# Kernel optimization log

Hardware: AMD Instinct MI355X
Metric: run time of the kernel (lower is better)

## Reference

```python
import jax, jax.numpy as jnp
import numpy as np

C = 512          # in_channels
N1 = 8192        # level-1 nodes
N2 = 131072      # level-2 nodes
N = 1 + N1 + N2  # total nodes (node 0 = root)
E = 1_000_000    # edges
STEP = 10        # ceil(1/ratio), ratio=0.1
K1 = (N1 + STEP - 1) // STEP   # 820 level-1 clusters
K2 = 4 * K1                    # max level-2 clusters (4 centers per parent)
M = 1 + K1 + K2                # coarse node count


def setup_inputs() -> dict:
    key = jax.random.key(0)
    ks = jax.random.split(key, 6)
    x = jax.random.normal(ks[0], (N, C), dtype=jnp.float32)
    edge_index = jax.random.randint(ks[1], (2, E), 0, N, dtype=jnp.int32)
    # fixed hierarchy layout: node 0 root, nodes 1..N1 level-1, rest level-2
    node_type = jnp.concatenate([jnp.zeros(1, jnp.int32),
                                 jnp.ones(N1, jnp.int32),
                                 jnp.full((N2,), 2, jnp.int32)])
    # tree: level-2 nodes point to a level-1 parent (global idx in [1, N1])
    tree = jax.random.randint(ks[2], (N,), 1, N1 + 1, dtype=jnp.int32)
    x_y_index = jax.random.uniform(ks[3], (N, 2), dtype=jnp.float32) * 100.0
    weight_1 = jax.random.normal(ks[4], (1, C), dtype=jnp.float32) * 0.04
    weight_2 = jax.random.normal(ks[5], (1, C), dtype=jnp.float32) * 0.04
    return {"x": x, "edge_index": edge_index, "node_type": node_type,
            "tree": tree, "x_y_index": x_y_index,
            "weight_1": weight_1, "weight_2": weight_2}


def _pair_dist(a, b):
    # a:[m,3], b:[n,3]; xy euclidean distance + |fitness diff| (euclidean_dist)
    dxy = jnp.sqrt(jnp.sum((a[:, None, :2] - b[None, :, :2]) ** 2, axis=-1))
    df = jnp.abs(a[:, None, 2] - b[None, :, 2])
    return dxy + df


def reference(x, edge_index, node_type, tree, x_y_index, weight_1, weight_2):
    x1, x2 = x[1:1 + N1], x[1 + N1:]
    xy1, xy2 = x_y_index[1:1 + N1], x_y_index[1 + N1:]

    # ---- level-1: fitness, threshold selection, cluster by nearest center ----
    f1 = jnp.tanh(jnp.sum(x1 * weight_1, axis=-1) / jnp.linalg.norm(weight_1))
    xyf1 = jnp.concatenate([xy1, f1[:, None]], axis=-1)          # [N1,3]
    order1 = jnp.argsort(f1)
    thr1 = order1[::STEP]                                        # [K1]
    d1 = _pair_dist(xyf1[thr1], xyf1)                            # [K1,N1]
    cluster_1 = jnp.argmin(d1, axis=0).astype(jnp.int32)         # [N1]

    # ---- level-2: fitness, 4 centers per parent cluster, nearest-center ----
    f2 = jnp.tanh(jnp.sum(x2 * weight_2, axis=-1) / jnp.linalg.norm(weight_2))
    xyf2 = jnp.concatenate([xy2, f2[:, None]], axis=-1)          # [N2,3]
    tree2 = tree[1 + N1:]
    parents = cluster_1[tree2 - jnp.min(tree2)]                  # [N2] in [0,K1)
    # pick 4 lowest-fitness members of each parent cluster as centers
    # (static-shape deterministic variant of random.sample over sorted fitness)
    comp_key = parents.astype(jnp.float32) * 4.0 + f2            # fitness in (-1,1)
    order2 = jnp.argsort(comp_key)
    p_sorted = parents[order2]
    counts = jax.ops.segment_sum(jnp.ones((N2,), jnp.int32), parents, K1)
    starts = jnp.concatenate([jnp.zeros(1, jnp.int32), jnp.cumsum(counts)[:-1]])
    rank = jnp.arange(N2, dtype=jnp.int32) - starts[p_sorted]
    row = jnp.where(rank < 4, p_sorted, K1)                      # overflow -> dummy row
    cand = jnp.full((K1 + 1, 4), -1, jnp.int32)
    cand = cand.at[row, jnp.clip(rank, 0, 3)].set(order2.astype(jnp.int32))[:K1]
    valid = cand >= 0                                            # [K1,4]
    cand_xyf = xyf2[jnp.where(valid, cand, 0)]                   # [K1,4,3]
    a = cand_xyf[parents]                                        # [N2,4,3]
    d2 = (jnp.sqrt(jnp.sum((a[..., :2] - xy2[:, None, :]) ** 2, axis=-1))
          + jnp.abs(a[..., 2] - f2[:, None]))
    d2 = jnp.where(valid[parents], d2, jnp.inf)
    local = jnp.argmin(d2, axis=1).astype(jnp.int32)             # [N2] in [0,4)
    cluster_2 = parents * 4 + local                              # [N2]

    # ---- merge cluster ids: [root | level-1 clusters | level-2 clusters] ----
    cluster = jnp.concatenate([jnp.zeros(1, jnp.int32),
                               cluster_1 + 1,
                               cluster_2 + 1 + K1])              # [N] in [0,M)

    # ---- scatter-mean pooling of features and coordinates ----
    cnt = jnp.maximum(jax.ops.segment_sum(jnp.ones((N, 1), x.dtype), cluster, M), 1.0)
    x_pool = jax.ops.segment_sum(x, cluster, M) / cnt            # [M,C]
    new_xy = jax.ops.segment_sum(x_y_index, cluster, M) / cnt    # [M,2]

    # ---- coarsen adjacency (self loops added on fine graph first) ----
    rows = jnp.concatenate([edge_index[0], jnp.arange(N, dtype=jnp.int32)])
    cols = jnp.concatenate([edge_index[1], jnp.arange(N, dtype=jnp.int32)])
    A = jnp.zeros((M, M), x.dtype).at[cluster[rows], cluster[cols]].add(1.0)

    new_node_type = jnp.concatenate([jnp.zeros(1, jnp.int32),
                                     jnp.ones(K1, jnp.int32),
                                     jnp.full((K2,), 2, jnp.int32)])
    new_tree = jnp.concatenate([jnp.full((1,), -1, jnp.int32),
                                jnp.zeros(K1, jnp.int32),
                                jnp.repeat(jnp.arange(1, K1 + 1, dtype=jnp.int32), 4)])
    fitness = jnp.concatenate([jnp.zeros(1, x.dtype), f1, f2])
    batch = jnp.zeros((M,), jnp.int32)
    return x_pool, A, batch, cluster, new_node_type, new_tree, fitness, new_xy
```

## Files before the change

kernel.cpp:

```cpp
#include <hip/hip_runtime.h>
#include <cstdint>
#include <cstddef>
#include <math.h>

#define C_     512
#define N1_    8192
#define N2_    131072
#define NTOT   139265
#define E_     1000000
#define K1_    820
#define K2_    3280
#define M_     4101
#define NB2    256
#define NBM    273

#define OFF_XPOOL   0ull
#define OFF_A       2099712ull
#define OFF_BATCH   18917913ull
#define OFF_CLUSTER 18922014ull
#define OFF_NNT     19061279ull
#define OFF_NTREE   19065380ull
#define OFF_FIT     19069481ull
#define OFF_NXY     19208746ull
#define OUT_TOTAL   19216948ull


__global__ void k_zero4(float4* __restrict__ p, long n4, float* __restrict__ tail, int ntail) {
    long i = (long)blockIdx.x * blockDim.x + threadIdx.x;
    long stride = (long)gridDim.x * blockDim.x;
    float4 z = make_float4(0.f, 0.f, 0.f, 0.f);
    for (; i < n4; i += stride) p[i] = z;
    if (blockIdx.x == 0 && threadIdx.x < ntail) tail[threadIdx.x] = 0.f;
}

__device__ __forceinline__ float pairwise_combine(float r) {
    float o;
    o = __shfl_xor(r, 1, 64);  r = __fadd_rn(r, o);
    o = __shfl_xor(r, 2, 64);  r = __fadd_rn(r, o);
    o = __shfl_xor(r, 4, 64);  r = __fadd_rn(r, o);
    o = __shfl_xor(r, 8, 64);  r = __fadd_rn(r, o);
    o = __shfl_xor(r, 16, 64); r = __fadd_rn(r, o);
    return r;
}

__global__ void k_norms(const float* __restrict__ w1, const float* __restrict__ w2,
                        float* __restrict__ norms) {
    __shared__ float buf[2][C_];
    int wv = threadIdx.x >> 6, lane = threadIdx.x & 63;
    const float* w = (wv == 0) ? w1 : w2;
    float4* b4 = (float4*)buf[wv];
    const float4* w4 = (const float4*)w;
    b4[lane] = w4[lane];
    b4[lane + 64] = w4[lane + 64];
    __syncthreads();
    float r = 0.f;
    if (lane < 32) {
        int base = (lane >> 3) * 128 + (lane & 7);
        float v = buf[wv][base];
        r = __fmul_rn(v, v);
        for (int i = 1; i < 16; ++i) {
            float u = buf[wv][base + 8 * i];
            r = __fadd_rn(r, __fmul_rn(u, u));
        }
    }
    r = pairwise_combine(r);
    if (lane == 0) norms[wv] = __fsqrt_rn(r);
}

__global__ void k_fit(const float* __restrict__ x, const float* __restrict__ w,
                      const float* __restrict__ norms, int normIdx,
                      int rowOff, int nRows, float* __restrict__ fs,
                      float* __restrict__ fitOut) {
    __shared__ float wbuf[C_];
    __shared__ float xbuf[4][C_];
    for (int j = threadIdx.x; j < C_; j += 256) wbuf[j] = w[j];
    int wv = threadIdx.x >> 6, lane = threadIdx.x & 63;
    int gw = blockIdx.x * 4 + wv;
    const float4* row = (const float4*)(x + (size_t)(rowOff + gw) * C_);
    float4* xb4 = (float4*)xbuf[wv];
    xb4[lane] = row[lane];
    xb4[lane + 64] = row[lane + 64];
    __syncthreads();
    float r = 0.f;
    if (lane < 32) {
        int base = (lane >> 3) * 128 + (lane & 7);
        r = __fmul_rn(xbuf[wv][base], wbuf[base]);
        for (int i = 1; i < 16; ++i) {
            int c = base + 8 * i;
            r = __fadd_rn(r, __fmul_rn(xbuf[wv][c], wbuf[c]));
        }
    }
    r = pairwise_combine(r);
    if (lane == 0) {
        float q = __fdiv_rn(r, norms[normIdx]);
        float f = (float)tanh((double)q);
        fs[gw] = f;
        fitOut[gw] = f;
    }
    (void)nRows;
}

#define RJ 512
__global__ void k_rank_partial(const float* __restrict__ f1s, int* __restrict__ rank) {
    __shared__ float buf[RJ];
    int i = blockIdx.x * 256 + threadIdx.x;
    int jbase = blockIdx.y * RJ;
    for (int j = threadIdx.x; j < RJ; j += 256) buf[j] = f1s[jbase + j];
    float fi = f1s[i];
    __syncthreads();
    int r = 0;
    #pragma unroll 8
    for (int j = 0; j < RJ; ++j) {
        float fj = buf[j];
        int jj = jbase + j;
        r += (int)((fj < fi) || (fj == fi && jj < i));
    }
    atomicAdd(&rank[i], r);
}

__global__ void k_thr_emit(const int* __restrict__ rank, int* __restrict__ thr1) {
    int i = blockIdx.x * blockDim.x + threadIdx.x;
    if (i >= N1_) return;
    int r = rank[i];
    if (r % 10 == 0) thr1[r / 10] = i;
}

__global__ void k_thr_gather(const int* __restrict__ thr1, const float* __restrict__ xy,
                             const float* __restrict__ f1s, float* __restrict__ thrXYF) {
    int k = blockIdx.x * blockDim.x + threadIdx.x;
    if (k >= K1_) return;
    int i = thr1[k];
    thrXYF[3 * k + 0] = xy[(size_t)(1 + i) * 2 + 0];
    thrXYF[3 * k + 1] = xy[(size_t)(1 + i) * 2 + 1];
    thrXYF[3 * k + 2] = f1s[i];
}

__device__ __forceinline__ float pair_dist_f32(float ax, float ay, float af,
                                               float bx, float by, float bf) {
    float dx = __fsub_rn(ax, bx);
    float dy = __fsub_rn(ay, by);
    float dx2 = __fmul_rn(dx, dx);
    float dy2 = __fmul_rn(dy, dy);
    float ss = __fadd_rn(dx2, dy2);
    float dxy = __fsqrt_rn(ss);
    float df = fabsf(__fsub_rn(af, bf));
    return __fadd_rn(dxy, df);
}

__global__ void k_cluster1(const float* __restrict__ xy, const float* __restrict__ f1s,
                           const float* __restrict__ thrXYF,
                           int* __restrict__ cluster1, int* __restrict__ clusterAll,
                           float* __restrict__ outCluster) {
    __shared__ float t[K1_ * 3];
    for (int j = threadIdx.x; j < K1_ * 3; j += blockDim.x) t[j] = thrXYF[j];
    __syncthreads();
    if (blockIdx.x == 0 && threadIdx.x == 0) { clusterAll[0] = 0; outCluster[0] = 0.0f; }
    int gw = blockIdx.x * (blockDim.x >> 6) + (threadIdx.x >> 6);
    int lane = threadIdx.x & 63;
    if (gw >= N1_) return;
    float xi = xy[(size_t)(1 + gw) * 2 + 0];
    float yi = xy[(size_t)(1 + gw) * 2 + 1];
    float fi = f1s[gw];
    float best = INFINITY; int bk = 0x7fffffff;
    for (int k = lane; k < K1_; k += 64) {
        float d = pair_dist_f32(t[3 * k + 0], t[3 * k + 1], t[3 * k + 2], xi, yi, fi);
        if (d < best || (d == best && k < bk)) { best = d; bk = k; }
    }
    for (int off = 32; off > 0; off >>= 1) {
        float ob = __shfl_down(best, off, 64);
        int ok = __shfl_down(bk, off, 64);
        if (ob < best || (ob == best && ok < bk)) { best = ob; bk = ok; }
    }
    if (lane == 0) {
        cluster1[gw] = bk;
        clusterAll[1 + gw] = bk + 1;
        outCluster[1 + gw] = (float)(bk + 1);
    }
}

__global__ void k_mintree(const int* __restrict__ tree, int* __restrict__ minTree) {
    int i = blockIdx.x * blockDim.x + threadIdx.x;
    if (i >= N2_) return;
    int v = tree[1 + N1_ + i];
    for (int off = 32; off > 0; off >>= 1) v = min(v, __shfl_down(v, off, 64));
    if ((threadIdx.x & 63) == 0) atomicMin(minTree, v);
}

__global__ void k_parents(const int* __restrict__ tree, const int* __restrict__ cluster1,
                          const int* __restrict__ minTree,
                          int* __restrict__ parents, int* __restrict__ countP) {
    int i = blockIdx.x * blockDim.x + threadIdx.x;
    if (i >= N2_) return;
    int p = cluster1[tree[1 + N1_ + i] - minTree[0]];
    parents[i] = p;
    atomicAdd(&countP[p], 1);
}

__global__ void k_scan(const int* __restrict__ cnt, int* __restrict__ start, int n) {
    __shared__ int partial[1024];
    int t = threadIdx.x;
    int per = (n + 1023) / 1024;
    int lo = t * per;
    int hi = lo + per; if (hi > n) hi = n;
    int s = 0;
    if (lo < n) for (int i = lo; i < hi; ++i) s += cnt[i];
    partial[t] = s;
    __syncthreads();
    for (int off = 1; off < 1024; off <<= 1) {
        int v = (t >= off) ? partial[t - off] : 0;
        __syncthreads();
        partial[t] += v;
        __syncthreads();
    }
    int base = (t > 0) ? partial[t - 1] : 0;
    if (lo < n) for (int i = lo; i < hi; ++i) { start[i] = base; base += cnt[i]; }
    if (t == 1023) start[n] = partial[1023];
}

__global__ void kA_count(const int* __restrict__ parents, int* __restrict__ bc) {
    __shared__ int hist[K1_];
    for (int j = threadIdx.x; j < K1_; j += 512) hist[j] = 0;
    __syncthreads();
    int i = blockIdx.x * 512 + threadIdx.x;
    atomicAdd(&hist[parents[i]], 1);
    __syncthreads();
    for (int j = threadIdx.x; j < K1_; j += 512) bc[(size_t)j * NB2 + blockIdx.x] = hist[j];
}

__global__ void kA_scan(const int* __restrict__ startP, int* __restrict__ bc) {
    int p = blockIdx.x * 256 + threadIdx.x;
    if (p >= K1_) return;
    int run = startP[p];
    int* row = bc + (size_t)p * NB2;
    for (int b = 0; b < NB2; ++b) { int t = row[b]; row[b] = run; run += t; }
}

__global__ void kA_place(const int* __restrict__ parents, const int* __restrict__ bc,
                         int* __restrict__ plist) {
    __shared__ int par[512];
    int i = blockIdx.x * 512 + threadIdx.x;
    int p = parents[i];
    par[threadIdx.x] = p;
    __syncthreads();
    int rank = 0;
    for (int j = 0; j < (int)threadIdx.x; ++j) rank += (par[j] == p);
    plist[bc[(size_t)p * NB2 + blockIdx.x] + rank] = i;
}

__global__ void kM_count(const int* __restrict__ clusterAll, int* __restrict__ bc) {
    __shared__ int hist[M_];
    for (int j = threadIdx.x; j < M_; j += 512) hist[j] = 0;
    __syncthreads();
    int i = blockIdx.x * 512 + threadIdx.x;
    if (i < NTOT) atomicAdd(&hist[clusterAll[i]], 1);
    __syncthreads();
    for (int j = threadIdx.x; j < M_; j += 512) bc[(size_t)j * NBM + blockIdx.x] = hist[j];
}

__global__ void kM_scan(const int* __restrict__ startM, int* __restrict__ bc) {
    int c = blockIdx.x * 256 + threadIdx.x;
    if (c >= M_) return;
    int run = startM[c];
    int* row = bc + (size_t)c * NBM;
    for (int b = 0; b < NBM; ++b) { int t = row[b]; row[b] = run; run += t; }
}

__global__ void kM_place(const int* __restrict__ clusterAll, const int* __restrict__ bc,
                         int* __restrict__ lst) {
    __shared__ int par[512];
    int i = blockIdx.x * 512 + threadIdx.x;
    int c = (i < NTOT) ? clusterAll[i] : -1;
    par[threadIdx.x] = c;
    __syncthreads();
    if (i >= NTOT) return;
    int rank = 0;
    for (int j = 0; j < (int)threadIdx.x; ++j) rank += (par[j] == c);
    lst[bc[(size_t)c * NBM + blockIdx.x] + rank] = i;
}

__global__ void k_top4(const int* __restrict__ startP, const int* __restrict__ plist,
                       const float* __restrict__ f2s, int* __restrict__ cand) {
    int p = blockIdx.x * (blockDim.x >> 6) + (threadIdx.x >> 6);
    int lane = threadIdx.x & 63;
    if (p >= K1_) return;
    int lo = startP[p], hi = startP[p + 1];
    float base = (float)(4 * p);
    float bk[4] = {INFINITY, INFINITY, INFINITY, INFINITY};
    int bi[4] = {-1, -1, -1, -1};
    for (int q = lo + lane; q < hi; q += 64) {
        int idx = plist[q];
        float key = __fadd_rn(base, f2s[idx]);
        for (int j = 0; j < 4; ++j) {
            bool less = (key < bk[j]) || (key == bk[j] && (unsigned)idx < (unsigned)bi[j]);
            if (less) {
                for (int r = 3; r > j; --r) { bk[r] = bk[r - 1]; bi[r] = bi[r - 1]; }
                bk[j] = key; bi[j] = idx;
                break;
            }
        }
    }
    for (int off = 1; off < 64; off <<= 1) {
        float ok_[4]; int oi[4];
        for (int j = 0; j < 4; ++j) {
            ok_[j] = __shfl_xor(bk[j], off, 64);
            oi[j]  = __shfl_xor(bi[j], off, 64);
        }
        float nk[4]; int ni[4];
        int ia = 0, ib = 0;
        for (int j = 0; j < 4; ++j) {
            bool takeA = (bk[ia] < ok_[ib]) ||
                         (bk[ia] == ok_[ib] && (unsigned)bi[ia] <= (unsigned)oi[ib]);
            if (takeA) { nk[j] = bk[ia]; ni[j] = bi[ia]; ++ia; }
            else       { nk[j] = ok_[ib]; ni[j] = oi[ib]; ++ib; }
        }
        for (int j = 0; j < 4; ++j) { bk[j] = nk[j]; bi[j] = ni[j]; }
    }
    if (lane == 0) {
        for (int j = 0; j < 4; ++j) cand[4 * p + j] = bi[j];
    }
}

__global__ void k_cluster2(const float* __restrict__ xy, const float* __restrict__ f2s,
                           const int* __restrict__ parents, const int* __restrict__ cand,
                           int* __restrict__ clusterAll, float* __restrict__ outCluster) {
    int i = blockIdx.x * blockDim.x + threadIdx.x;
    if (i >= N2_) return;
    int p = parents[i];
    float xi = xy[(size_t)(1 + N1_ + i) * 2 + 0];
    float yi = xy[(size_t)(1 + N1_ + i) * 2 + 1];
    float fi = f2s[i];
    float best = INFINITY; int bj = 0;
    for (int j = 0; j < 4; ++j) {
        int cidx = cand[4 * p + j];
        float d;
        if (cidx < 0) {
            d = INFINITY;
        } else {
            float ax = xy[(size_t)(1 + N1_ + cidx) * 2 + 0];
            float ay = xy[(size_t)(1 + N1_ + cidx) * 2 + 1];
            float af = f2s[cidx];
            d = pair_dist_f32(ax, ay, af, xi, yi, fi);
        }
        if (d < best) { best = d; bj = j; }
    }
    int c2 = p * 4 + bj;
    clusterAll[1 + N1_ + i] = c2 + 1 + K1_;
    outCluster[1 + N1_ + i] = (float)(c2 + 1 + K1_);
}

__global__ void k_countM(const int* __restrict__ clusterAll, int* __restrict__ cntM) {
    int i = blockIdx.x * blockDim.x + threadIdx.x;
    if (i >= NTOT) return;
    atomicAdd(&cntM[clusterAll[i]], 1);
}

__global__ void k_pool(const float* __restrict__ x, const float* __restrict__ xy,
                       const int* __restrict__ startM, const int* __restrict__ clusterList,
                       float* __restrict__ out) {
    int m = blockIdx.x;
    int lo = startM[m], hi = startM[m + 1];
    int t = threadIdx.x;
    double s0 = 0.0, s1 = 0.0, sx = 0.0, sy = 0.0;
    for (int q = lo; q < hi; ++q) {
        int n0 = clusterList[q];
        const float2* r0 = (const float2*)(x + (size_t)n0 * C_);
        float2 a = r0[t];
        s0 += (double)a.x; s1 += (double)a.y;
        if (t == 0) sx += (double)xy[(size_t)n0 * 2 + 0];
        if (t == 1) sy += (double)xy[(size_t)n0 * 2 + 1];
    }
    double cnt = (double)((hi - lo) > 0 ? (hi - lo) : 1);
    float2* xp = (float2*)(out + OFF_XPOOL + (size_t)m * C_);
    xp[t] = make_float2((float)(s0 / cnt), (float)(s1 / cnt));
    if (t == 0) out[OFF_NXY + 2 * (size_t)m + 0] = (float)(sx / cnt);
    if (t == 1) out[OFF_NXY + 2 * (size_t)m + 1] = (float)(sy / cnt);
}

__global__ void k_edges(const int* __restrict__ ei, const int* __restrict__ clusterAll,
                        float* __restrict__ A) {
    int e = blockIdx.x * blockDim.x + threadIdx.x;
    if (e >= E_) return;
    int r = clusterAll[ei[e]];
    int c = clusterAll[ei[E_ + e]];
    atomicAdd(&A[(size_t)r * M_ + c], 1.0f);
}

__global__ void k_selfloops(const int* __restrict__ clusterAll, float* __restrict__ A) {
    int i = blockIdx.x * blockDim.x + threadIdx.x;
    if (i >= NTOT) return;
    int c = clusterAll[i];
    atomicAdd(&A[(size_t)c * M_ + c], 1.0f);
}

__global__ void k_trivial(float* __restrict__ out) {
    int i = blockIdx.x * blockDim.x + threadIdx.x;
    if (i >= M_) return;
    out[OFF_NNT + i] = (i == 0) ? 0.0f : (i <= K1_ ? 1.0f : 2.0f);
    out[OFF_NTREE + i] = (i == 0) ? -1.0f : (i <= K1_ ? 0.0f : (float)(1 + (i - 1 - K1_) / 4));
    out[OFF_BATCH + i] = 0.0f;
    if (i == 0) out[OFF_FIT] = 0.0f;
}

extern "C" void kernel_launch(void* const* d_in, const int* in_sizes, int n_in,
                              void* d_out, int out_size, void* d_ws, size_t ws_size,
                              hipStream_t stream) {
    const float* x    = (const float*)d_in[0];
    const int*   ei   = (const int*)d_in[1];
    const int*   tree = (const int*)d_in[3];
    const float* xy   = (const float*)d_in[4];
    const float* w1   = (const float*)d_in[5];
    const float* w2   = (const float*)d_in[6];
    float* out = (float*)d_out;

    char* p = (char*)d_ws;
    auto alloc = [&](size_t nbytes) -> char* {
        char* r = p;
        p += (nbytes + 255) & ~(size_t)255;
        return r;
    };
    float*  f1s        = (float*)alloc((size_t)N1_ * 4);
    float*  f2s        = (float*)alloc((size_t)N2_ * 4);
    float*  norms      = (float*)alloc(16);
    int*    thr1       = (int*)alloc((size_t)K1_ * 4);
    float*  thrXYF     = (float*)alloc((size_t)K1_ * 3 * 4);
    int*    cluster1   = (int*)alloc((size_t)N1_ * 4);
    int*    clusterAll = (int*)alloc((size_t)NTOT * 4);
    int*    parentsA   = (int*)alloc((size_t)N2_ * 4);
    int*    plist      = (int*)alloc((size_t)N2_ * 4);
    int*    clusterLst = (int*)alloc((size_t)NTOT * 4);
    int*    startP     = (int*)alloc((size_t)(K1_ + 1) * 4);
    int*    startM     = (int*)alloc((size_t)(M_ + 1) * 4);
    int*    bcP        = (int*)alloc((size_t)K1_ * NB2 * 4);
    int*    bcM        = (int*)alloc((size_t)M_ * NBM * 4);
    size_t zeroInts = (size_t)(K1_ + M_ + N1_);
    char*   zeroBlk    = alloc(zeroInts * 4);
    int*    countP     = (int*)zeroBlk;
    int*    cntM       = countP + K1_;
    int*    rankArr    = cntM + M_;
    int*    cand       = (int*)alloc((size_t)K1_ * 4 * 4);
    int*    minTree    = (int*)alloc(4);

    hipMemsetAsync(zeroBlk, 0, zeroInts * 4, stream);
    hipMemsetAsync(minTree, 0x7F, 4, stream);

    {
        long nA = (long)M_ * M_;
        long n4 = nA / 4;
        int ntail = (int)(nA - n4 * 4);
        float* A = out + OFF_A;
        k_zero4<<<4096, 256, 0, stream>>>((float4*)A, n4, A + n4 * 4, ntail);
    }

    k_norms<<<1, 128, 0, stream>>>(w1, w2, norms);
    k_fit<<<N1_ / 4, 256, 0, stream>>>(x, w1, norms, 0, 1, N1_, f1s, out + OFF_FIT + 1);
    k_fit<<<N2_ / 4, 256, 0, stream>>>(x, w2, norms, 1, 1 + N1_, N2_, f2s, out + OFF_FIT + 1 + N1_);
    {
        dim3 g(N1_ / 256, N1_ / RJ);
        k_rank_partial<<<g, 256, 0, stream>>>(f1s, rankArr);
    }
    k_thr_emit<<<N1_ / 256, 256, 0, stream>>>(rankArr, thr1);
    k_thr_gather<<<(K1_ + 255) / 256, 256, 0, stream>>>(thr1, xy, f1s, thrXYF);
    k_cluster1<<<N1_ / 4, 256, 0, stream>>>(xy, f1s, thrXYF, cluster1, clusterAll,
                                            out + OFF_CLUSTER);
    k_mintree<<<N2_ / 256, 256, 0, stream>>>(tree, minTree);
    k_parents<<<N2_ / 256, 256, 0, stream>>>(tree, cluster1, minTree, parentsA, countP);
    k_scan<<<1, 1024, 0, stream>>>(countP, startP, K1_);
    kA_count<<<NB2, 512, 0, stream>>>(parentsA, bcP);
    kA_scan<<<(K1_ + 255) / 256, 256, 0, stream>>>(startP, bcP);
    kA_place<<<NB2, 512, 0, stream>>>(parentsA, bcP, plist);
    k_top4<<<(K1_ + 3) / 4, 256, 0, stream>>>(startP, plist, f2s, cand);
    k_cluster2<<<N2_ / 256, 256, 0, stream>>>(xy, f2s, parentsA, cand, clusterAll,
                                              out + OFF_CLUSTER);
    k_countM<<<(NTOT + 255) / 256, 256, 0, stream>>>(clusterAll, cntM);
    k_scan<<<1, 1024, 0, stream>>>(cntM, startM, M_);
    kM_count<<<NBM, 512, 0, stream>>>(clusterAll, bcM);
    kM_scan<<<(M_ + 255) / 256, 256, 0, stream>>>(startM, bcM);
    kM_place<<<NBM, 512, 0, stream>>>(clusterAll, bcM, clusterLst);
    k_pool<<<M_, 256, 0, stream>>>(x, xy, startM, clusterLst, out);
    k_edges<<<(E_ + 255) / 256, 256, 0, stream>>>(ei, clusterAll, out + OFF_A);
    k_selfloops<<<(NTOT + 255) / 256, 256, 0, stream>>>(clusterAll, out + OFF_A);
    k_trivial<<<(M_ + 255) / 256, 256, 0, stream>>>(out);
}
```

Baseline: 835.3 us.

## Fuse small kernels and widen pooling loads to cut launches

Several small kernels are folded into neighbours. The weight-norm computation moves into the fitness kernel, and the threshold emit and gather become one kernel. Cluster counting moves into the cluster kernels as atomics, self-loops are merged into the edge kernel, and the trivial outputs are written by the zero kernel. The fitness kernel now handles two rows per wave, and pooling uses float4 loads with 128 threads processing two nodes per iteration. The goal is less launch overhead and wider memory accesses. The cost is extra atomics in the cluster kernels and redundant norm work in every fitness wave.

```diff
diff --git a/kernel.cpp b/kernel.cpp
--- a/kernel.cpp
+++ b/kernel.cpp
@@ -25,12 +25,19 @@
 #define OUT_TOTAL   19216948ull
 
 
-__global__ void k_zero4(float4* __restrict__ p, long n4, float* __restrict__ tail, int ntail) {
+__global__ void k_zero4(float4* __restrict__ p, long n4, float* __restrict__ tail, int ntail,
+                        float* __restrict__ out) {
     long i = (long)blockIdx.x * blockDim.x + threadIdx.x;
     long stride = (long)gridDim.x * blockDim.x;
     float4 z = make_float4(0.f, 0.f, 0.f, 0.f);
-    for (; i < n4; i += stride) p[i] = z;
+    for (long k = i; k < n4; k += stride) p[k] = z;
     if (blockIdx.x == 0 && threadIdx.x < ntail) tail[threadIdx.x] = 0.f;
+    if (i < M_) {
+        out[OFF_NNT + i] = (i == 0) ? 0.0f : (i <= K1_ ? 1.0f : 2.0f);
+        out[OFF_NTREE + i] = (i == 0) ? -1.0f : (i <= K1_ ? 0.0f : (float)(1 + (i - 1 - K1_) / 4));
+        out[OFF_BATCH + i] = 0.0f;
+        if (i == 0) out[OFF_FIT] = 0.0f;
+    }
 }
 
 __device__ __forceinline__ float pairwise_combine(float r) {
@@ -43,61 +50,45 @@
     return r;
 }
 
-__global__ void k_norms(const float* __restrict__ w1, const float* __restrict__ w2,
-                        float* __restrict__ norms) {
-    __shared__ float buf[2][C_];
-    int wv = threadIdx.x >> 6, lane = threadIdx.x & 63;
-    const float* w = (wv == 0) ? w1 : w2;
-    float4* b4 = (float4*)buf[wv];
-    const float4* w4 = (const float4*)w;
-    b4[lane] = w4[lane];
-    b4[lane + 64] = w4[lane + 64];
-    __syncthreads();
-    float r = 0.f;
-    if (lane < 32) {
-        int base = (lane >> 3) * 128 + (lane & 7);
-        float v = buf[wv][base];
-        r = __fmul_rn(v, v);
-        for (int i = 1; i < 16; ++i) {
-            float u = buf[wv][base + 8 * i];
-            r = __fadd_rn(r, __fmul_rn(u, u));
-        }
-    }
-    r = pairwise_combine(r);
-    if (lane == 0) norms[wv] = __fsqrt_rn(r);
-}
-
 __global__ void k_fit(const float* __restrict__ x, const float* __restrict__ w,
-                      const float* __restrict__ norms, int normIdx,
-                      int rowOff, int nRows, float* __restrict__ fs,
-                      float* __restrict__ fitOut) {
+                      int rowOff, float* __restrict__ fs, float* __restrict__ fitOut) {
     __shared__ float wbuf[C_];
-    __shared__ float xbuf[4][C_];
+    __shared__ float xbuf[8][C_];
     for (int j = threadIdx.x; j < C_; j += 256) wbuf[j] = w[j];
     int wv = threadIdx.x >> 6, lane = threadIdx.x & 63;
-    int gw = blockIdx.x * 4 + wv;
-    const float4* row = (const float4*)(x + (size_t)(rowOff + gw) * C_);
-    float4* xb4 = (float4*)xbuf[wv];
-    xb4[lane] = row[lane];
-    xb4[lane + 64] = row[lane + 64];
-    __syncthreads();
-    float r = 0.f;
-    if (lane < 32) {
-        int base = (lane >> 3) * 128 + (lane & 7);
-        r = __fmul_rn(xbuf[wv][base], wbuf[base]);
-        for (int i = 1; i < 16; ++i) {
-            int c = base + 8 * i;
-            r = __fadd_rn(r, __fmul_rn(xbuf[wv][c], wbuf[c]));
-        }
-    }
+    int rowA = blockIdx.x * 8 + wv * 2;
+    const float4* rA = (const float4*)(x + (size_t)(rowOff + rowA) * C_);
+    const float4* rB = (const float4*)(x + (size_t)(rowOff + rowA + 1) * C_);
+    float4* xa = (float4*)xbuf[wv * 2];
+    float4* xb = (float4*)xbuf[wv * 2 + 1];
+    xa[lane] = rA[lane];
+    xa[lane + 64] = rA[lane + 64];
+    xb[lane] = rB[lane];
+    xb[lane + 64] = rB[lane + 64];
+    __syncthreads();
+    int hl = lane & 31;
+    int base = (hl >> 3) * 128 + (hl & 7);
+    const float* xr = xbuf[wv * 2 + (lane >> 5)];
+    float nv = wbuf[base];
+    float nr = __fmul_rn(nv, nv);
+    float r = __fmul_rn(xr[base], wbuf[base]);
+    #pragma unroll
+    for (int i = 1; i < 16; ++i) {
+        int c = base + 8 * i;
+        float u = wbuf[c];
+        nr = __fadd_rn(nr, __fmul_rn(u, u));
+        r = __fadd_rn(r, __fmul_rn(xr[c], u));
+    }
+    nr = pairwise_combine(nr);
     r = pairwise_combine(r);
-    if (lane == 0) {
-        float q = __fdiv_rn(r, norms[normIdx]);
+    if (hl == 0) {
+        float nrm = __fsqrt_rn(nr);
+        float q = __fdiv_rn(r, nrm);
         float f = (float)tanh((double)q);
+        int gw = rowA + (lane >> 5);
         fs[gw] = f;
         fitOut[gw] = f;
     }
-    (void)nRows;
 }
 
 #define RJ 512
@@ -118,21 +109,17 @@
     atomicAdd(&rank[i], r);
 }
 
-__global__ void k_thr_emit(const int* __restrict__ rank, int* __restrict__ thr1) {
+__global__ void k_thr(const int* __restrict__ rank, const float* __restrict__ xy,
+                      const float* __restrict__ f1s, float* __restrict__ thrXYF) {
     int i = blockIdx.x * blockDim.x + threadIdx.x;
     if (i >= N1_) return;
     int r = rank[i];
-    if (r % 10 == 0) thr1[r / 10] = i;
-}
-
-__global__ void k_thr_gather(const int* __restrict__ thr1, const float* __restrict__ xy,
-                             const float* __restrict__ f1s, float* __restrict__ thrXYF) {
-    int k = blockIdx.x * blockDim.x + threadIdx.x;
-    if (k >= K1_) return;
-    int i = thr1[k];
-    thrXYF[3 * k + 0] = xy[(size_t)(1 + i) * 2 + 0];
-    thrXYF[3 * k + 1] = xy[(size_t)(1 + i) * 2 + 1];
-    thrXYF[3 * k + 2] = f1s[i];
+    if (r % 10 == 0) {
+        int k = r / 10;
+        thrXYF[3 * k + 0] = xy[(size_t)(1 + i) * 2 + 0];
+        thrXYF[3 * k + 1] = xy[(size_t)(1 + i) * 2 + 1];
+        thrXYF[3 * k + 2] = f1s[i];
+    }
 }
 
 __device__ __forceinline__ float pair_dist_f32(float ax, float ay, float af,
@@ -150,11 +137,14 @@
 __global__ void k_cluster1(const float* __restrict__ xy, const float* __restrict__ f1s,
                            const float* __restrict__ thrXYF,
                            int* __restrict__ cluster1, int* __restrict__ clusterAll,
-                           float* __restrict__ outCluster) {
+                           float* __restrict__ outCluster, int* __restrict__ cntM) {
     __shared__ float t[K1_ * 3];
     for (int j = threadIdx.x; j < K1_ * 3; j += blockDim.x) t[j] = thrXYF[j];
     __syncthreads();
-    if (blockIdx.x == 0 && threadIdx.x == 0) { clusterAll[0] = 0; outCluster[0] = 0.0f; }
+    if (blockIdx.x == 0 && threadIdx.x == 0) {
+        clusterAll[0] = 0; outCluster[0] = 0.0f;
+        atomicAdd(&cntM[0], 1);
+    }
     int gw = blockIdx.x * (blockDim.x >> 6) + (threadIdx.x >> 6);
     int lane = threadIdx.x & 63;
     if (gw >= N1_) return;
@@ -175,6 +165,7 @@
         cluster1[gw] = bk;
         clusterAll[1 + gw] = bk + 1;
         outCluster[1 + gw] = (float)(bk + 1);
+        atomicAdd(&cntM[bk + 1], 1);
     }
 }
 
@@ -322,7 +313,8 @@
 
 __global__ void k_cluster2(const float* __restrict__ xy, const float* __restrict__ f2s,
                            const int* __restrict__ parents, const int* __restrict__ cand,
-                           int* __restrict__ clusterAll, float* __restrict__ outCluster) {
+                           int* __restrict__ clusterAll, float* __restrict__ outCluster,
+                           int* __restrict__ cntM) {
     int i = blockIdx.x * blockDim.x + threadIdx.x;
     if (i >= N2_) return;
     int p = parents[i];
@@ -344,14 +336,10 @@
         if (d < best) { best = d; bj = j; }
     }
     int c2 = p * 4 + bj;
-    clusterAll[1 + N1_ + i] = c2 + 1 + K1_;
-    outCluster[1 + N1_ + i] = (float)(c2 + 1 + K1_);
-}
-
-__global__ void k_countM(const int* __restrict__ clusterAll, int* __restrict__ cntM) {
-    int i = blockIdx.x * blockDim.x + threadIdx.x;
-    if (i >= NTOT) return;
-    atomicAdd(&cntM[clusterAll[i]], 1);
+    int c = c2 + 1 + K1_;
+    clusterAll[1 + N1_ + i] = c;
+    outCluster[1 + N1_ + i] = (float)c;
+    atomicAdd(&cntM[c], 1);
 }
 
 __global__ void k_pool(const float* __restrict__ x, const float* __restrict__ xy,
@@ -360,45 +348,47 @@
     int m = blockIdx.x;
     int lo = startM[m], hi = startM[m + 1];
     int t = threadIdx.x;
-    double s0 = 0.0, s1 = 0.0, sx = 0.0, sy = 0.0;
-    for (int q = lo; q < hi; ++q) {
+    double s0 = 0.0, s1 = 0.0, s2 = 0.0, s3 = 0.0, sx = 0.0, sy = 0.0;
+    int q = lo;
+    for (; q + 1 < hi; q += 2) {
         int n0 = clusterList[q];
-        const float2* r0 = (const float2*)(x + (size_t)n0 * C_);
-        float2 a = r0[t];
-        s0 += (double)a.x; s1 += (double)a.y;
+        int n1 = clusterList[q + 1];
+        float4 a = ((const float4*)(x + (size_t)n0 * C_))[t];
+        float4 b = ((const float4*)(x + (size_t)n1 * C_))[t];
+        s0 += (double)a.x; s1 += (double)a.y; s2 += (double)a.z; s3 += (double)a.w;
+        s0 += (double)b.x; s1 += (double)b.y; s2 += (double)b.z; s3 += (double)b.w;
+        if (t == 0) sx += (double)xy[(size_t)n0 * 2 + 0] + (double)xy[(size_t)n1 * 2 + 0];
+        if (t == 1) sy += (double)xy[(size_t)n0 * 2 + 1] + (double)xy[(size_t)n1 * 2 + 1];
+    }
+    if (q < hi) {
+        int n0 = clusterList[q];
+        float4 a = ((const float4*)(x + (size_t)n0 * C_))[t];
+        s0 += (double)a.x; s1 += (double)a.y; s2 += (double)a.z; s3 += (double)a.w;
         if (t == 0) sx += (double)xy[(size_t)n0 * 2 + 0];
         if (t == 1) sy += (double)xy[(size_t)n0 * 2 + 1];
     }
     double cnt = (double)((hi - lo) > 0 ? (hi - lo) : 1);
-    float2* xp = (float2*)(out + OFF_XPOOL + (size_t)m * C_);
-    xp[t] = make_float2((float)(s0 / cnt), (float)(s1 / cnt));
+    float4* xp = (float4*)(out + OFF_XPOOL + (size_t)m * C_);
+    xp[t] = make_float4((float)(s0 / cnt), (float)(s1 / cnt),
+                        (float)(s2 / cnt), (float)(s3 / cnt));
     if (t == 0) out[OFF_NXY + 2 * (size_t)m + 0] = (float)(sx / cnt);
     if (t == 1) out[OFF_NXY + 2 * (size_t)m + 1] = (float)(sy / cnt);
 }
 
 __global__ void k_edges(const int* __restrict__ ei, const int* __restrict__ clusterAll,
                         float* __restrict__ A) {
-    int e = blockIdx.x * blockDim.x + threadIdx.x;
-    if (e >= E_) return;
-    int r = clusterAll[ei[e]];
-    int c = clusterAll[ei[E_ + e]];
-    atomicAdd(&A[(size_t)r * M_ + c], 1.0f);
-}
-
-__global__ void k_selfloops(const int* __restrict__ clusterAll, float* __restrict__ A) {
     int i = blockIdx.x * blockDim.x + threadIdx.x;
-    if (i >= NTOT) return;
-    int c = clusterAll[i];
-    atomicAdd(&A[(size_t)c * M_ + c], 1.0f);
-}
-
-__global__ void k_trivial(float* __restrict__ out) {
-    int i = blockIdx.x * blockDim.x + threadIdx.x;
-    if (i >= M_) return;
-    out[OFF_NNT + i] = (i == 0) ? 0.0f : (i <= K1_ ? 1.0f : 2.0f);
-    out[OFF_NTREE + i] = (i == 0) ? -1.0f : (i <= K1_ ? 0.0f : (float)(1 + (i - 1 - K1_) / 4));
-    out[OFF_BATCH + i] = 0.0f;
-    if (i == 0) out[OFF_FIT] = 0.0f;
+    if (i < E_) {
+        int r = clusterAll[ei[i]];
+        int c = clusterAll[ei[E_ + i]];
+        atomicAdd(&A[(size_t)r * M_ + c], 1.0f);
+    } else {
+        int n = i - E_;
+        if (n < NTOT) {
+            int c = clusterAll[n];
+            atomicAdd(&A[(size_t)c * M_ + c], 1.0f);
+        }
+    }
 }
 
 extern "C" void kernel_launch(void* const* d_in, const int* in_sizes, int n_in,
@@ -420,8 +410,6 @@
     };
     float*  f1s        = (float*)alloc((size_t)N1_ * 4);
     float*  f2s        = (float*)alloc((size_t)N2_ * 4);
-    float*  norms      = (float*)alloc(16);
-    int*    thr1       = (int*)alloc((size_t)K1_ * 4);
     float*  thrXYF     = (float*)alloc((size_t)K1_ * 3 * 4);
     int*    cluster1   = (int*)alloc((size_t)N1_ * 4);
     int*    clusterAll = (int*)alloc((size_t)NTOT * 4);
@@ -448,20 +436,18 @@
         long n4 = nA / 4;
         int ntail = (int)(nA - n4 * 4);
         float* A = out + OFF_A;
-        k_zero4<<<4096, 256, 0, stream>>>((float4*)A, n4, A + n4 * 4, ntail);
-    }
-
-    k_norms<<<1, 128, 0, stream>>>(w1, w2, norms);
-    k_fit<<<N1_ / 4, 256, 0, stream>>>(x, w1, norms, 0, 1, N1_, f1s, out + OFF_FIT + 1);
-    k_fit<<<N2_ / 4, 256, 0, stream>>>(x, w2, norms, 1, 1 + N1_, N2_, f2s, out + OFF_FIT + 1 + N1_);
+        k_zero4<<<4096, 256, 0, stream>>>((float4*)A, n4, A + n4 * 4, ntail, out);
+    }
+
+    k_fit<<<N1_ / 8, 256, 0, stream>>>(x, w1, 1, f1s, out + OFF_FIT + 1);
+    k_fit<<<N2_ / 8, 256, 0, stream>>>(x, w2, 1 + N1_, f2s, out + OFF_FIT + 1 + N1_);
     {
         dim3 g(N1_ / 256, N1_ / RJ);
         k_rank_partial<<<g, 256, 0, stream>>>(f1s, rankArr);
     }
-    k_thr_emit<<<N1_ / 256, 256, 0, stream>>>(rankArr, thr1);
-    k_thr_gather<<<(K1_ + 255) / 256, 256, 0, stream>>>(thr1, xy, f1s, thrXYF);
+    k_thr<<<N1_ / 256, 256, 0, stream>>>(rankArr, xy, f1s, thrXYF);
     k_cluster1<<<N1_ / 4, 256, 0, stream>>>(xy, f1s, thrXYF, cluster1, clusterAll,
-                                            out + OFF_CLUSTER);
+                                            out + OFF_CLUSTER, cntM);
     k_mintree<<<N2_ / 256, 256, 0, stream>>>(tree, minTree);
     k_parents<<<N2_ / 256, 256, 0, stream>>>(tree, cluster1, minTree, parentsA, countP);
     k_scan<<<1, 1024, 0, stream>>>(countP, startP, K1_);
@@ -470,14 +456,11 @@
     kA_place<<<NB2, 512, 0, stream>>>(parentsA, bcP, plist);
     k_top4<<<(K1_ + 3) / 4, 256, 0, stream>>>(startP, plist, f2s, cand);
     k_cluster2<<<N2_ / 256, 256, 0, stream>>>(xy, f2s, parentsA, cand, clusterAll,
-                                              out + OFF_CLUSTER);
-    k_countM<<<(NTOT + 255) / 256, 256, 0, stream>>>(clusterAll, cntM);
+                                              out + OFF_CLUSTER, cntM);
     k_scan<<<1, 1024, 0, stream>>>(cntM, startM, M_);
     kM_count<<<NBM, 512, 0, stream>>>(clusterAll, bcM);
     kM_scan<<<(M_ + 255) / 256, 256, 0, stream>>>(startM, bcM);
     kM_place<<<NBM, 512, 0, stream>>>(clusterAll, bcM, clusterLst);
-    k_pool<<<M_, 256, 0, stream>>>(x, xy, startM, clusterLst, out);
-    k_edges<<<(E_ + 255) / 256, 256, 0, stream>>>(ei, clusterAll, out + OFF_A);
-    k_selfloops<<<(NTOT + 255) / 256, 256, 0, stream>>>(clusterAll, out + OFF_A);
-    k_trivial<<<(M_ + 255) / 256, 256, 0, stream>>>(out);
-}
+    k_pool<<<M_, 128, 0, stream>>>(x, xy, startM, clusterLst, out);
+    k_edges<<<(E_ + NTOT + 255) / 256, 256, 0, stream>>>(ei, clusterAll, out + OFF_A);
+}
```

Result: faster. 801.4 us (-4.1%).
